# Kernel tuning notes

Measured on AMD Instinct MI355X. Metric: run time of the kernel, lower is better.

The kernel has to match this reference:

```python
import jax, jax.numpy as jnp
import numpy as np

T, B, I, H = 512, 64, 1024, 1024


def setup_inputs() -> dict:
    key = jax.random.key(0)
    ks = jax.random.split(key, 7)
    s = 1.0 / np.sqrt(H)  # torch LSTMCell default init scale
    return {
        "x": jax.random.normal(ks[0], (T, B, I), dtype=jnp.float32),
        "h0": jax.random.normal(ks[1], (B, H), dtype=jnp.float32),
        "c0": jax.random.normal(ks[2], (B, H), dtype=jnp.float32),
        "W_ih": jax.random.normal(ks[3], (4 * H, I), dtype=jnp.float32) * s,
        "W_hh": jax.random.normal(ks[4], (4 * H, H), dtype=jnp.float32) * s,
        "b_ih": jax.random.normal(ks[5], (4 * H,), dtype=jnp.float32) * s,
        "b_hh": jax.random.normal(ks[6], (4 * H,), dtype=jnp.float32) * s,
    }


def _reverse_lstm(x, h0, c0, W_ih, W_hh, b_ih, b_hh):
    def step(carry, x_t):
        h, c = carry
        # gates: [B, 4H]
        gates = x_t @ W_ih.T + b_ih + h @ W_hh.T + b_hh
        i_g, f_g, g_g, o_g = jnp.split(gates, 4, axis=-1)
        i_g = jax.nn.sigmoid(i_g)
        f_g = jax.nn.sigmoid(f_g)
        g_g = jnp.tanh(g_g)
        o_g = jax.nn.sigmoid(o_g)
        c_new = f_g * c + i_g * g_g
        h_new = o_g * jnp.tanh(c_new)
        return (h_new, c_new), h_new

    # reverse=True: scan from last timestep to first; ys[i] aligns with x[i],
    # matching the torch code's reverse(unbind) -> loop -> reverse(outputs).
    (hT, cT), ys = jax.lax.scan(step, (h0, c0), x, reverse=True)
    return ys, (hT, cT)


def reference(x, h0, c0, W_ih, W_hh, b_ih, b_hh):
    return _reverse_lstm(x, h0, c0, W_ih, W_hh, b_ih, b_hh)
```

## Files before the change

### kernel.cpp

```cpp
#include <hip/hip_runtime.h>

#define TT 512
#define BB 64
#define HH 1024
#define G4 4096

typedef _Float16 h8 __attribute__((ext_vector_type(8)));
typedef float f4 __attribute__((ext_vector_type(4)));
typedef unsigned long long u64;

#define BAR_LGKM() do {                                      \
  asm volatile("s_waitcnt lgkmcnt(0)" ::: "memory");         \
  __builtin_amdgcn_sched_barrier(0);                         \
  __builtin_amdgcn_s_barrier();                              \
  __builtin_amdgcn_sched_barrier(0);                         \
} while (0)

#define BAR_VM0() do {                                       \
  asm volatile("s_waitcnt vmcnt(0)" ::: "memory");           \
  __builtin_amdgcn_sched_barrier(0);                         \
  __builtin_amdgcn_s_barrier();                              \
  __builtin_amdgcn_sched_barrier(0);                         \
} while (0)

__device__ __forceinline__ float sigm_fast(float x) {
  return __builtin_amdgcn_rcpf(1.f + __expf(-x));
}
__device__ __forceinline__ float tanh_fast(float x) {
  float cx = fminf(15.f, fmaxf(-15.f, x));
  float e = __expf(2.f * cx);
  return (e - 1.f) * __builtin_amdgcn_rcpf(e + 1.f);
}


__global__ void k_conv_wih(const float* __restrict__ w, _Float16* __restrict__ o) {
  int i = blockIdx.x * 256 + threadIdx.x;
  const f4* src = (const f4*)w + (size_t)i * 2;
  f4 a = src[0], b = src[1];
  h8 r;
  r[0] = (_Float16)a[0]; r[1] = (_Float16)a[1]; r[2] = (_Float16)a[2]; r[3] = (_Float16)a[3];
  r[4] = (_Float16)b[0]; r[5] = (_Float16)b[1]; r[6] = (_Float16)b[2]; r[7] = (_Float16)b[3];
  *(h8*)(o + (size_t)i * 8) = r;
}

__global__ void k_shuf_whh(const float* __restrict__ w, _Float16* __restrict__ o) {
  int cidx = blockIdx.x * 256 + threadIdx.x;
  int b = cidx >> 6;
  int lid = cidx & 63;
  int n = (b >> 5) * 16 + (lid & 15);
  int k0 = (b & 31) * 32 + (lid >> 4) * 8;
  const float* src = w + (size_t)n * HH + k0;
  h8 r;
  #pragma unroll
  for (int j = 0; j < 8; ++j) r[j] = (_Float16)src[j];
  *(h8*)(o + (size_t)b * 512 + lid * 8) = r;
}

__global__ void k_bsum(const float* __restrict__ bi, const float* __restrict__ bh,
                       float* __restrict__ o) {
  int i = blockIdx.x * 256 + threadIdx.x;
  o[i] = bi[i] + bh[i];
}

__global__ void k_prep(const float* __restrict__ h0, _Float16* __restrict__ hbuf,
                       unsigned* __restrict__ bar) {
  int i = blockIdx.x * 256 + threadIdx.x;
  hbuf[i] = (_Float16)h0[i];
  if (i < 2048) bar[i] = 0u;
}

__global__ __launch_bounds__(256) void k_gemm_gx(
    const float* __restrict__ x, const _Float16* __restrict__ wih,
    const float* __restrict__ bsum, _Float16* __restrict__ gxL) {
  __shared__ _Float16 As[128 * 40];
  __shared__ _Float16 Bs[128 * 40];
  const int bid = blockIdx.x;
  const int m0 = (bid >> 5) * 128;
  const int n0 = (bid & 31) * 128;
  const int tid = threadIdx.x;
  const int w = tid >> 6, l = tid & 63, q = l >> 4, lj = l & 15;
  const int wm = (w >> 1) * 64, wn = (w & 1) * 64;
  const int lrow = tid >> 1;
  const int lcol = (tid & 1) * 16;

  f4 z = {0.f, 0.f, 0.f, 0.f};
  f4 acc[4][4];
  #pragma unroll
  for (int i2 = 0; i2 < 4; ++i2)
    #pragma unroll
    for (int j2 = 0; j2 < 4; ++j2) acc[i2][j2] = z;

  for (int kt = 0; kt < 32; ++kt) {
    const int k0 = kt * 32;
    const float* xp = x + (size_t)(m0 + lrow) * HH + k0 + lcol;
    f4 a0 = ((const f4*)xp)[0];
    f4 a1 = ((const f4*)xp)[1];
    f4 a2 = ((const f4*)xp)[2];
    f4 a3 = ((const f4*)xp)[3];
    const _Float16* bp = wih + (size_t)(n0 + lrow) * HH + k0 + lcol;
    h8 b0 = ((const h8*)bp)[0];
    h8 b1 = ((const h8*)bp)[1];
    h8 lo, hi;
    lo[0] = (_Float16)a0[0]; lo[1] = (_Float16)a0[1]; lo[2] = (_Float16)a0[2]; lo[3] = (_Float16)a0[3];
    lo[4] = (_Float16)a1[0]; lo[5] = (_Float16)a1[1]; lo[6] = (_Float16)a1[2]; lo[7] = (_Float16)a1[3];
    hi[0] = (_Float16)a2[0]; hi[1] = (_Float16)a2[1]; hi[2] = (_Float16)a2[2]; hi[3] = (_Float16)a2[3];
    hi[4] = (_Float16)a3[0]; hi[5] = (_Float16)a3[1]; hi[6] = (_Float16)a3[2]; hi[7] = (_Float16)a3[3];
    __syncthreads();
    *(h8*)&As[lrow * 40 + lcol] = lo;
    *(h8*)&As[lrow * 40 + lcol + 8] = hi;
    *(h8*)&Bs[lrow * 40 + lcol] = b0;
    *(h8*)&Bs[lrow * 40 + lcol + 8] = b1;
    __syncthreads();
    h8 af[4], bf[4];
    #pragma unroll
    for (int mt = 0; mt < 4; ++mt) af[mt] = *(h8*)&As[(wm + mt * 16 + lj) * 40 + q * 8];
    #pragma unroll
    for (int nt = 0; nt < 4; ++nt) bf[nt] = *(h8*)&Bs[(wn + nt * 16 + lj) * 40 + q * 8];
    #pragma unroll
    for (int mt = 0; mt < 4; ++mt)
      #pragma unroll
      for (int nt = 0; nt < 4; ++nt)
        acc[mt][nt] = __builtin_amdgcn_mfma_f32_16x16x32_f16(af[mt], bf[nt], acc[mt][nt], 0, 0, 0);
  }
  const int tt = (m0 + wm) >> 6;
  #pragma unroll
  for (int nt = 0; nt < 4; ++nt) {
    int nbase = n0 + wn + nt * 16;
    float bv = bsum[nbase + lj];
    int wq = nbase >> 10;
    int sq = (nbase >> 4) & 63;
    _Float16* dst = gxL + (((size_t)tt * 4 + wq) * 64 + sq) * 1024 + (q * 16 + lj) * 16;
    #pragma unroll
    for (int mt = 0; mt < 4; ++mt) {
      union { _Float16 h[4]; u64 u; } pk;
      #pragma unroll
      for (int r = 0; r < 4; ++r) pk.h[r] = (_Float16)(acc[mt][nt][r] + bv);
      *(u64*)(dst + mt * 4) = pk.u;
    }
  }
}

__global__ __launch_bounds__(256, 1) void k_lstm_seq(
    const _Float16* __restrict__ gxL, const _Float16* __restrict__ wsh,
    const float* __restrict__ c0, float* __restrict__ out,
    _Float16* __restrict__ hbuf, unsigned* __restrict__ bar) {
  __shared__ _Float16 hs[2][64 * 136];
  __shared__ float gbuf[4 * 64 * 20];
  __shared__ float cs[64 * 20];
  const int tid = threadIdx.x;
  const int s = blockIdx.x;
  const int w = tid >> 6;
  const int l = tid & 63;
  const int q = l >> 4;
  const int lj = l & 15;
  const int em = tid >> 2;
  const int ec = (tid & 3) * 4;
  const int c0r = s >> 3;

  #pragma unroll
  for (int u = 0; u < 4; ++u) {
    int e = u * 256 + tid;
    cs[(e >> 4) * 20 + (e & 15)] = c0[(size_t)(e >> 4) * HH + s * 16 + (e & 15)];
  }

  for (int ii = 0; ii < TT; ++ii) {
    const int t = TT - 1 - ii;
    const _Float16* __restrict__ hcur = hbuf + (size_t)(ii & 1) * (BB * HH);
    _Float16* __restrict__ hnxt = hbuf + (size_t)((ii + 1) & 1) * (BB * HH);
    const unsigned tgt = (unsigned)ii;

    const _Float16* gxb = gxL + (((size_t)t * 4 + w) * 64 + s) * 1024 + (size_t)l * 16;
    h8 g0 = *(const h8*)gxb;
    h8 g1 = *(const h8*)(gxb + 8);

    u64 rdy = 0;
    auto wait_chunk = [&](int c) {
      while (((rdy >> (c * 8)) & 0xFFull) != 0xFFull) {
        unsigned v = __hip_atomic_load(&bar[l * 32], __ATOMIC_RELAXED,
                                       __HIP_MEMORY_SCOPE_AGENT);
        rdy = __ballot(v >= tgt);
        if (((rdy >> (c * 8)) & 0xFFull) == 0xFFull) break;
        __builtin_amdgcn_s_sleep(1);
      }
    };
    auto load_chunk = [&](int c, u64* dst) {
      #pragma unroll
      for (int u = 0; u < 8; ++u) {
        int e = u * 256 + tid;
        dst[u] = __hip_atomic_load(
            (const u64*)&hcur[(size_t)(e >> 5) * HH + c * 128 + (e & 31) * 4],
            __ATOMIC_RELAXED, __HIP_MEMORY_SCOPE_AGENT);
      }
    };

    f4 z = {0.f, 0.f, 0.f, 0.f};
    f4 acc[4];
    #pragma unroll
    for (int mt = 0; mt < 4; ++mt) acc[mt] = z;

    u64 pre[3][8];
    wait_chunk(c0r);             load_chunk(c0r, pre[0]);
    wait_chunk((c0r + 1) & 7);   load_chunk((c0r + 1) & 7, pre[1]);
    wait_chunk((c0r + 2) & 7);   load_chunk((c0r + 2) & 7, pre[2]);

    #pragma unroll
    for (int ck = 0; ck < 8; ++ck) {
      const int ckx = (ck + c0r) & 7;
      u64* cur = pre[ck % 3];
      #pragma unroll
      for (int u = 0; u < 8; ++u) {
        int e = u * 256 + tid;
        *(u64*)&hs[ck & 1][(e >> 5) * 136 + (e & 31) * 4] = cur[u];
      }
      BAR_LGKM();
      if (ck < 5) {
        int cn = (ck + 3 + c0r) & 7;
        wait_chunk(cn);
        load_chunk(cn, cur);
      }
      #pragma unroll
      for (int kk = 0; kk < 4; ++kk) {
        int blk = (w * 64 + s) * 32 + ckx * 4 + kk;
        h8 bfr = *(const h8*)&wsh[(size_t)blk * 512 + l * 8];
        #pragma unroll
        for (int mt = 0; mt < 4; ++mt) {
          h8 afr = *(const h8*)&hs[ck & 1][(mt * 16 + lj) * 136 + kk * 32 + q * 8];
          acc[mt] = __builtin_amdgcn_mfma_f32_16x16x32_f16(afr, bfr, acc[mt], 0, 0, 0);
        }
      }
    }
    #pragma unroll
    for (int mt = 0; mt < 4; ++mt) {
      #pragma unroll
      for (int r = 0; r < 4; ++r) {
        int m = mt * 16 + q * 4 + r;
        float gxv = (float)((mt < 2 ? g0 : g1)[(mt & 1) * 4 + r]);
        gbuf[(w * 64 + m) * 20 + lj] = acc[mt][r] + gxv;
      }
    }
    BAR_LGKM();
    f4 gi4 = *(f4*)&gbuf[(0 * 64 + em) * 20 + ec];
    f4 gf4 = *(f4*)&gbuf[(1 * 64 + em) * 20 + ec];
    f4 gg4 = *(f4*)&gbuf[(2 * 64 + em) * 20 + ec];
    f4 go4 = *(f4*)&gbuf[(3 * 64 + em) * 20 + ec];
    f4 cold = *(f4*)&cs[em * 20 + ec];
    f4 hn4, cn4;
    #pragma unroll
    for (int j = 0; j < 4; ++j) {
      float iv = sigm_fast(gi4[j]);
      float fv = sigm_fast(gf4[j]);
      float gv = tanh_fast(gg4[j]);
      float ov = sigm_fast(go4[j]);
      float cn = fv * cold[j] + iv * gv;
      cn4[j] = cn;
      hn4[j] = ov * tanh_fast(cn);
    }
    *(f4*)&cs[em * 20 + ec] = cn4;
    union { _Float16 h[4]; u64 u; } pk;
    #pragma unroll
    for (int j = 0; j < 4; ++j) pk.h[j] = (_Float16)hn4[j];
    __hip_atomic_store((u64*)&hnxt[(size_t)em * HH + s * 16 + ec], pk.u,
                       __ATOMIC_RELAXED, __HIP_MEMORY_SCOPE_AGENT);
    BAR_VM0();
    if (tid == 0)
      __hip_atomic_store(&bar[s * 32], (unsigned)(ii + 1), __ATOMIC_RELAXED,
                         __HIP_MEMORY_SCOPE_AGENT);
    *(f4*)&out[((size_t)t * BB + em) * HH + s * 16 + ec] = hn4;
    if (t == 0) {
      *(f4*)&out[(size_t)TT * BB * HH + (size_t)em * HH + s * 16 + ec] = hn4;
      *(f4*)&out[(size_t)TT * BB * HH + (size_t)BB * HH + (size_t)em * HH + s * 16 + ec] = cn4;
    }
  }
}

extern "C" void kernel_launch(void* const* d_in, const int* in_sizes, int n_in,
                              void* d_out, int out_size, void* d_ws, size_t ws_size,
                              hipStream_t stream) {
  const float* x    = (const float*)d_in[0];
  const float* h0   = (const float*)d_in[1];
  const float* c0   = (const float*)d_in[2];
  const float* W_ih = (const float*)d_in[3];
  const float* W_hh = (const float*)d_in[4];
  const float* b_ih = (const float*)d_in[5];
  const float* b_hh = (const float*)d_in[6];
  float* out = (float*)d_out;

  char* ws = (char*)d_ws;
  size_t off = 0;
  auto take = [&](size_t bytes) -> void* {
    void* p = ws + off;
    off = (off + bytes + 255) & ~(size_t)255;
    return p;
  };
  _Float16* gxL   = (_Float16*)take((size_t)TT * BB * G4 * 2);
  _Float16* wih_h = (_Float16*)take((size_t)G4 * HH * 2);
  _Float16* wsh   = (_Float16*)take((size_t)G4 * HH * 2);
  float*    bsum  = (float*)take((size_t)G4 * 4);
  _Float16* hbuf  = (_Float16*)take((size_t)2 * BB * HH * 2);
  unsigned* bar   = (unsigned*)take(64 * 32 * 4);
  if (off > ws_size) return;

  k_conv_wih<<<2048, 256, 0, stream>>>(W_ih, wih_h);
  k_shuf_whh<<<2048, 256, 0, stream>>>(W_hh, wsh);
  k_bsum<<<16, 256, 0, stream>>>(b_ih, b_hh, bsum);
  k_prep<<<256, 256, 0, stream>>>(h0, hbuf, bar);
  k_gemm_gx<<<8192, 256, 0, stream>>>(x, wih_h, bsum, gxL);
  k_lstm_seq<<<64, 256, 0, stream>>>(gxL, wsh, c0, out, hbuf, bar);
}
```

Before: 4.893 ms.

## Replace per-chunk readiness polling with end-of-step grid barrier and prefetch W_hh fragments

```diff
diff --git a/kernel.cpp b/kernel.cpp
--- a/kernel.cpp
+++ b/kernel.cpp
@@ -9,19 +9,7 @@
 typedef float f4 __attribute__((ext_vector_type(4)));
 typedef unsigned long long u64;
 
-#define BAR_LGKM() do {                                      \
-  asm volatile("s_waitcnt lgkmcnt(0)" ::: "memory");         \
-  __builtin_amdgcn_sched_barrier(0);                         \
-  __builtin_amdgcn_s_barrier();                              \
-  __builtin_amdgcn_sched_barrier(0);                         \
-} while (0)
-
-#define BAR_VM0() do {                                       \
-  asm volatile("s_waitcnt vmcnt(0)" ::: "memory");           \
-  __builtin_amdgcn_sched_barrier(0);                         \
-  __builtin_amdgcn_s_barrier();                              \
-  __builtin_amdgcn_sched_barrier(0);                         \
-} while (0)
+#define BARX() asm volatile("s_waitcnt lgkmcnt(0)\ns_barrier" ::: "memory")
 
 __device__ __forceinline__ float sigm_fast(float x) {
   return __builtin_amdgcn_rcpf(1.f + __expf(-x));
@@ -155,7 +143,6 @@
   const int lj = l & 15;
   const int em = tid >> 2;
   const int ec = (tid & 3) * 4;
-  const int c0r = s >> 3;
 
   #pragma unroll
   for (int u = 0; u < 4; ++u) {
@@ -167,66 +154,71 @@
     const int t = TT - 1 - ii;
     const _Float16* __restrict__ hcur = hbuf + (size_t)(ii & 1) * (BB * HH);
     _Float16* __restrict__ hnxt = hbuf + (size_t)((ii + 1) & 1) * (BB * HH);
-    const unsigned tgt = (unsigned)ii;
 
     const _Float16* gxb = gxL + (((size_t)t * 4 + w) * 64 + s) * 1024 + (size_t)l * 16;
     h8 g0 = *(const h8*)gxb;
     h8 g1 = *(const h8*)(gxb + 8);
 
-    u64 rdy = 0;
-    auto wait_chunk = [&](int c) {
-      while (((rdy >> (c * 8)) & 0xFFull) != 0xFFull) {
-        unsigned v = __hip_atomic_load(&bar[l * 32], __ATOMIC_RELAXED,
-                                       __HIP_MEMORY_SCOPE_AGENT);
-        rdy = __ballot(v >= tgt);
-        if (((rdy >> (c * 8)) & 0xFFull) == 0xFFull) break;
-        __builtin_amdgcn_s_sleep(1);
-      }
-    };
-    auto load_chunk = [&](int c, u64* dst) {
-      #pragma unroll
-      for (int u = 0; u < 8; ++u) {
-        int e = u * 256 + tid;
-        dst[u] = __hip_atomic_load(
-            (const u64*)&hcur[(size_t)(e >> 5) * HH + c * 128 + (e & 31) * 4],
-            __ATOMIC_RELAXED, __HIP_MEMORY_SCOPE_AGENT);
-      }
-    };
+    u64 preA[8], preB[8];
+    #pragma unroll
+    for (int u = 0; u < 8; ++u) {
+      int e = u * 256 + tid;
+      preA[u] = __hip_atomic_load(
+          (const u64*)&hcur[(size_t)(e >> 5) * HH + 0 * 128 + (e & 31) * 4],
+          __ATOMIC_RELAXED, __HIP_MEMORY_SCOPE_AGENT);
+    }
+    #pragma unroll
+    for (int u = 0; u < 8; ++u) {
+      int e = u * 256 + tid;
+      preB[u] = __hip_atomic_load(
+          (const u64*)&hcur[(size_t)(e >> 5) * HH + 1 * 128 + (e & 31) * 4],
+          __ATOMIC_RELAXED, __HIP_MEMORY_SCOPE_AGENT);
+    }
+    h8 bcur[4];
+    #pragma unroll
+    for (int kk = 0; kk < 4; ++kk)
+      bcur[kk] = *(const h8*)&wsh[(size_t)((w * 64 + s) * 32 + kk) * 512 + l * 8];
 
     f4 z = {0.f, 0.f, 0.f, 0.f};
     f4 acc[4];
     #pragma unroll
     for (int mt = 0; mt < 4; ++mt) acc[mt] = z;
 
-    u64 pre[3][8];
-    wait_chunk(c0r);             load_chunk(c0r, pre[0]);
-    wait_chunk((c0r + 1) & 7);   load_chunk((c0r + 1) & 7, pre[1]);
-    wait_chunk((c0r + 2) & 7);   load_chunk((c0r + 2) & 7, pre[2]);
-
     #pragma unroll
     for (int ck = 0; ck < 8; ++ck) {
-      const int ckx = (ck + c0r) & 7;
-      u64* cur = pre[ck % 3];
+      u64* cur = (ck & 1) ? preB : preA;
       #pragma unroll
       for (int u = 0; u < 8; ++u) {
         int e = u * 256 + tid;
         *(u64*)&hs[ck & 1][(e >> 5) * 136 + (e & 31) * 4] = cur[u];
       }
-      BAR_LGKM();
-      if (ck < 5) {
-        int cn = (ck + 3 + c0r) & 7;
-        wait_chunk(cn);
-        load_chunk(cn, cur);
+      h8 bnext[4];
+      if (ck < 7) {
+        #pragma unroll
+        for (int kk = 0; kk < 4; ++kk)
+          bnext[kk] = *(const h8*)&wsh[(size_t)((w * 64 + s) * 32 + (ck + 1) * 4 + kk) * 512 + l * 8];
+      }
+      BARX();
+      if (ck < 6) {
+        #pragma unroll
+        for (int u = 0; u < 8; ++u) {
+          int e = u * 256 + tid;
+          cur[u] = __hip_atomic_load(
+              (const u64*)&hcur[(size_t)(e >> 5) * HH + (ck + 2) * 128 + (e & 31) * 4],
+              __ATOMIC_RELAXED, __HIP_MEMORY_SCOPE_AGENT);
+        }
       }
       #pragma unroll
       for (int kk = 0; kk < 4; ++kk) {
-        int blk = (w * 64 + s) * 32 + ckx * 4 + kk;
-        h8 bfr = *(const h8*)&wsh[(size_t)blk * 512 + l * 8];
         #pragma unroll
         for (int mt = 0; mt < 4; ++mt) {
-          h8 afr = *(const h8*)&hs[ck & 1][(mt * 16 + lj) * 136 + kk * 32 + q * 8];
-          acc[mt] = __builtin_amdgcn_mfma_f32_16x16x32_f16(afr, bfr, acc[mt], 0, 0, 0);
+          h8 afr = *(h8*)&hs[ck & 1][(mt * 16 + lj) * 136 + kk * 32 + q * 8];
+          acc[mt] = __builtin_amdgcn_mfma_f32_16x16x32_f16(afr, bcur[kk], acc[mt], 0, 0, 0);
         }
+      }
+      if (ck < 7) {
+        #pragma unroll
+        for (int kk = 0; kk < 4; ++kk) bcur[kk] = bnext[kk];
       }
     }
     #pragma unroll
@@ -238,7 +230,7 @@
         gbuf[(w * 64 + m) * 20 + lj] = acc[mt][r] + gxv;
       }
     }
-    BAR_LGKM();
+    __syncthreads();
     f4 gi4 = *(f4*)&gbuf[(0 * 64 + em) * 20 + ec];
     f4 gf4 = *(f4*)&gbuf[(1 * 64 + em) * 20 + ec];
     f4 gg4 = *(f4*)&gbuf[(2 * 64 + em) * 20 + ec];
@@ -261,10 +253,19 @@
     for (int j = 0; j < 4; ++j) pk.h[j] = (_Float16)hn4[j];
     __hip_atomic_store((u64*)&hnxt[(size_t)em * HH + s * 16 + ec], pk.u,
                        __ATOMIC_RELAXED, __HIP_MEMORY_SCOPE_AGENT);
-    BAR_VM0();
+    __syncthreads();
     if (tid == 0)
       __hip_atomic_store(&bar[s * 32], (unsigned)(ii + 1), __ATOMIC_RELAXED,
                          __HIP_MEMORY_SCOPE_AGENT);
+    if (ii + 1 < TT) {
+      const unsigned tgt = (unsigned)(ii + 1);
+      while (true) {
+        unsigned v = __hip_atomic_load(&bar[l * 32], __ATOMIC_RELAXED,
+                                       __HIP_MEMORY_SCOPE_AGENT);
+        if (__all(v >= tgt)) break;
+        __builtin_amdgcn_s_sleep(1);
+      }
+    }
     *(f4*)&out[((size_t)t * BB + em) * HH + s * 16 + ec] = hn4;
     if (t == 0) {
       *(f4*)&out[(size_t)TT * BB * HH + (size_t)em * HH + s * 16 + ec] = hn4;
```

Result: faster. 3.987 ms (-18.5%).
